# Kernel tuning notes

Measured on AMD Instinct MI355X. Metric: run time of the kernel, lower is better.

The kernel has to match this reference:

```python
import jax, jax.numpy as jnp
import numpy as np

# Concrete segmented-polynomial instance (uniform 1d):
N = 8192      # nodes (rows of input 0 and of the indexed output)
E = 16384     # edges (batch dim of input 1 and of the per-edge product)
S = 16        # segments per operand (buffer_num_segments, same for all 3 operands)
EXT = 64      # operand_extent (uniform segment shape)
P = 2048      # num_paths of the single operation


def setup_inputs() -> dict:
    key = jax.random.key(0)
    k0, k1, k2, k3, k4, k5 = jax.random.split(key, 6)
    x = jax.random.normal(k0, (N, S * EXT), dtype=jnp.float32)          # node features
    y = jax.random.normal(k1, (E, S * EXT), dtype=jnp.float32)          # edge features
    idx_in = jax.random.randint(k2, (E,), 0, N, dtype=jnp.int32)        # gather index for input 0
    idx_out = jax.random.randint(k3, (E,), 0, N, dtype=jnp.int32)       # scatter index for output 0
    path_indices = jax.random.randint(k4, (P, 3), 0, S, dtype=jnp.int32)  # (i_x, j_y, k_out) per path
    path_coefficients = jax.random.normal(k5, (P,), dtype=jnp.float32)
    return {
        "x": x, "y": y,
        "idx_in": idx_in, "idx_out": idx_out,
        "path_indices": path_indices,
        "path_coefficients": path_coefficients,
    }


def reference(x, y, idx_in, idx_out, path_indices, path_coefficients):
    # Dense path-coefficient tensor C[k, i, j]: duplicate paths accumulate,
    # missing (k,i,j) triples are zero. This is the math-dtype (fp32) contraction
    # the uniform-1d kernel performs over segments of equal extent.
    C = jnp.zeros((S, S, S), dtype=x.dtype).at[
        path_indices[:, 2], path_indices[:, 0], path_indices[:, 1]
    ].add(path_coefficients)

    xr = x.reshape(N, S, EXT)[idx_in]   # gather (BATCH_DIM_INDEXED input): [E, S, EXT]
    yr = y.reshape(E, S, EXT)           # batched input:                    [E, S, EXT]

    # out_e[e, k, c] = sum_{i,j} C[k,i,j] * xr[e,i,c] * yr[e,j,c]
    out_e = jnp.einsum('kij,eic,ejc->ekc', C, xr, yr)

    # scatter-add (BATCH_DIM_INDEXED output) into N output rows
    out = jnp.zeros((N, S, EXT), dtype=x.dtype).at[idx_out].add(out_e)
    return out.reshape(N, S * EXT)
```

## Files before the change

### kernel.cpp

```cpp
#include <hip/hip_runtime.h>
#include <hip/hip_bf16.h>

#define N_NODES 8192
#define E_EDGES 16384
#define S_SEG   16
#define EXT     64
#define P_PATHS 2048
#define ROW     (S_SEG * EXT)
#define TE      4

typedef __bf16 bf16x8 __attribute__((ext_vector_type(8)));
typedef float  f32x4  __attribute__((ext_vector_type(4)));
typedef int    int4v  __attribute__((ext_vector_type(4)));

__device__ __forceinline__ int pack_bf16(float a, float b) {
#if __has_builtin(__builtin_amdgcn_cvt_pk_bf16_f32)
    auto r = __builtin_amdgcn_cvt_pk_bf16_f32(a, b);
    return __builtin_bit_cast(int, r);
#else
    unsigned ua = __float_as_uint(a), ub = __float_as_uint(b);
    ua = (ua + 0x7fffu + ((ua >> 16) & 1u)) >> 16;
    ub = (ub + 0x7fffu + ((ub >> 16) & 1u)) & 0xffff0000u;
    return (int)(ua | ub);
#endif
}

__global__ void build_C(const int* __restrict__ pidx,
                        const float* __restrict__ pcoef,
                        unsigned short* __restrict__ Cmat) {
    __shared__ float sC[S_SEG * S_SEG * S_SEG];
    const int tid = threadIdx.x;
    for (int i = tid; i < S_SEG * S_SEG * S_SEG; i += 256) sC[i] = 0.f;
    __syncthreads();
    for (int p = tid; p < P_PATHS; p += 256) {
        int i = pidx[3 * p + 0];
        int j = pidx[3 * p + 1];
        int k = pidx[3 * p + 2];
        atomicAdd(&sC[(k * S_SEG + i) * S_SEG + j], pcoef[p]);
    }
    __syncthreads();
    for (int idx = tid; idx < S_SEG * S_SEG * S_SEG; idx += 256) {
        unsigned u = __float_as_uint(sC[idx]);
        u = (u + 0x7fffu + ((u >> 16) & 1u)) >> 16;
        Cmat[idx] = (unsigned short)u;
    }
}

__global__ __launch_bounds__(256) void seg_poly(
        const float* __restrict__ x, const float* __restrict__ y,
        const int* __restrict__ idx_in, const int* __restrict__ idx_out,
        const unsigned short* __restrict__ Cmat, float* __restrict__ out) {
    __shared__ __attribute__((aligned(16))) float sx[TE][ROW];
    __shared__ __attribute__((aligned(16))) float sy[TE][ROW];

    const int tid  = threadIdx.x;
    const int lane = tid & 63;
    const int wv   = tid >> 6;
    const int quad = lane >> 4;
    const int c    = wv * 16 + (lane & 15);

    int4v afrag[8];
    {
        const int m = lane & 15;
        const unsigned short* base = Cmat + m * 256 + quad * 8;
#pragma unroll
        for (int kk = 0; kk < 8; ++kk)
            afrag[kk] = *(const int4v*)(base + kk * 32);
    }

    const int e0 = blockIdx.x * TE;

#pragma unroll
    for (int t = 0; t < TE; ++t) {
        const int e = e0 + t;
        const float4* xs = (const float4*)(x + (size_t)idx_in[e] * ROW);
        const float4* ys = (const float4*)(y + (size_t)e * ROW);
        ((float4*)sx[t])[tid] = xs[tid];
        ((float4*)sy[t])[tid] = ys[tid];
    }
    __syncthreads();

#pragma unroll
    for (int t = 0; t < TE; ++t) {
        const int e = e0 + t;

        const int jb = (quad & 1) * 8;
        float yv[8];
#pragma unroll
        for (int jr = 0; jr < 8; ++jr) yv[jr] = sy[t][(jb + jr) * EXT + c];

        const int ih = quad >> 1;
        f32x4 acc = {0.f, 0.f, 0.f, 0.f};
#pragma unroll
        for (int kk = 0; kk < 8; ++kk) {
            const float xc = sx[t][(kk * 2 + ih) * EXT + c];
            int4v bi;
            bi[0] = pack_bf16(xc * yv[0], xc * yv[1]);
            bi[1] = pack_bf16(xc * yv[2], xc * yv[3]);
            bi[2] = pack_bf16(xc * yv[4], xc * yv[5]);
            bi[3] = pack_bf16(xc * yv[6], xc * yv[7]);
            acc = __builtin_amdgcn_mfma_f32_16x16x32_bf16(
                __builtin_bit_cast(bf16x8, afrag[kk]),
                __builtin_bit_cast(bf16x8, bi), acc, 0, 0, 0);
        }

        float* ob = out + (size_t)idx_out[e] * ROW;
#pragma unroll
        for (int r = 0; r < 4; ++r)
            atomicAdd(ob + (quad * 4 + r) * EXT + c, acc[r]);
    }
}

extern "C" void kernel_launch(void* const* d_in, const int* in_sizes, int n_in,
                              void* d_out, int out_size, void* d_ws, size_t ws_size,
                              hipStream_t stream) {
    const float* x        = (const float*)d_in[0];
    const float* y        = (const float*)d_in[1];
    const int*   idx_in   = (const int*)d_in[2];
    const int*   idx_out  = (const int*)d_in[3];
    const int*   pidx     = (const int*)d_in[4];
    const float* pcoef    = (const float*)d_in[5];
    float* out            = (float*)d_out;
    unsigned short* Cmat  = (unsigned short*)d_ws;

    hipMemsetAsync(d_out, 0, (size_t)out_size * sizeof(float), stream);

    build_C<<<1, 256, 0, stream>>>(pidx, pcoef, Cmat);
    seg_poly<<<E_EDGES / TE, 256, 0, stream>>>(x, y, idx_in, idx_out, Cmat, out);
}
```

Measured before the change: 182.1 us.

## Replace atomic scatter with CSR-sorted per-node accumulation and fp16 MFMA

```diff
diff --git a/kernel.cpp b/kernel.cpp
--- a/kernel.cpp
+++ b/kernel.cpp
@@ -7,30 +7,26 @@
 #define EXT     64
 #define P_PATHS 2048
 #define ROW     (S_SEG * EXT)
-#define TE      4
 
-typedef __bf16 bf16x8 __attribute__((ext_vector_type(8)));
-typedef float  f32x4  __attribute__((ext_vector_type(4)));
-typedef int    int4v  __attribute__((ext_vector_type(4)));
+typedef _Float16 f16x8  __attribute__((ext_vector_type(8)));
+typedef _Float16 half2v __attribute__((ext_vector_type(2)));
+typedef float    f32x4  __attribute__((ext_vector_type(4)));
 
-__device__ __forceinline__ int pack_bf16(float a, float b) {
-#if __has_builtin(__builtin_amdgcn_cvt_pk_bf16_f32)
-    auto r = __builtin_amdgcn_cvt_pk_bf16_f32(a, b);
-    return __builtin_bit_cast(int, r);
-#else
-    unsigned ua = __float_as_uint(a), ub = __float_as_uint(b);
-    ua = (ua + 0x7fffu + ((ua >> 16) & 1u)) >> 16;
-    ub = (ub + 0x7fffu + ((ub >> 16) & 1u)) & 0xffff0000u;
-    return (int)(ua | ub);
-#endif
-}
+#define WS_CMAT  0
+#define WS_HIST  8192
+#define WS_CURS  40960
+#define WS_ROWS  73728
+#define WS_ELIST 106512
 
-__global__ void build_C(const int* __restrict__ pidx,
-                        const float* __restrict__ pcoef,
-                        unsigned short* __restrict__ Cmat) {
+__global__ void prep(const int* __restrict__ pidx, const float* __restrict__ pcoef,
+                     _Float16* __restrict__ Cmat, int* __restrict__ hist) {
+    const int tid = threadIdx.x;
+    if (blockIdx.x < 32) {
+        hist[blockIdx.x * 256 + tid] = 0;
+        return;
+    }
     __shared__ float sC[S_SEG * S_SEG * S_SEG];
-    const int tid = threadIdx.x;
-    for (int i = tid; i < S_SEG * S_SEG * S_SEG; i += 256) sC[i] = 0.f;
+    for (int i = tid; i < 4096; i += 256) sC[i] = 0.f;
     __syncthreads();
     for (int p = tid; p < P_PATHS; p += 256) {
         int i = pidx[3 * p + 0];
@@ -39,92 +35,148 @@
         atomicAdd(&sC[(k * S_SEG + i) * S_SEG + j], pcoef[p]);
     }
     __syncthreads();
-    for (int idx = tid; idx < S_SEG * S_SEG * S_SEG; idx += 256) {
-        unsigned u = __float_as_uint(sC[idx]);
-        u = (u + 0x7fffu + ((u >> 16) & 1u)) >> 16;
-        Cmat[idx] = (unsigned short)u;
-    }
+    for (int i = tid; i < 4096; i += 256) Cmat[i] = (_Float16)sC[i];
 }
 
-__global__ __launch_bounds__(256) void seg_poly(
+__global__ void hist_k(const int* __restrict__ idx_out, int* __restrict__ hist) {
+    const int e = blockIdx.x * 256 + threadIdx.x;
+    atomicAdd(&hist[idx_out[e]], 1);
+}
+
+__global__ __launch_bounds__(256) void scan_k(const int* __restrict__ hist,
+                                              int* __restrict__ rows,
+                                              int* __restrict__ cursor) {
+    __shared__ int part[256];
+    const int t = threadIdx.x;
+    const int base = t * 32;
+    int loc[32];
+    int s = 0;
+#pragma unroll
+    for (int i = 0; i < 32; ++i) { loc[i] = s; s += hist[base + i]; }
+    part[t] = s;
+    __syncthreads();
+    for (int off = 1; off < 256; off <<= 1) {
+        int v = part[t];
+        int u = (t >= off) ? part[t - off] : 0;
+        __syncthreads();
+        part[t] = v + u;
+        __syncthreads();
+    }
+    const int excl = (t == 0) ? 0 : part[t - 1];
+#pragma unroll
+    for (int i = 0; i < 32; ++i) {
+        int v = excl + loc[i];
+        rows[base + i] = v;
+        cursor[base + i] = v;
+    }
+    if (t == 255) rows[N_NODES] = part[255];
+}
+
+__global__ void scatter_k(const int* __restrict__ idx_out, int* __restrict__ cursor,
+                          int* __restrict__ elist) {
+    const int e = blockIdx.x * 256 + threadIdx.x;
+    const int pos = atomicAdd(&cursor[idx_out[e]], 1);
+    elist[pos] = e;
+}
+
+__global__ __launch_bounds__(256) void seg_poly_node(
         const float* __restrict__ x, const float* __restrict__ y,
-        const int* __restrict__ idx_in, const int* __restrict__ idx_out,
-        const unsigned short* __restrict__ Cmat, float* __restrict__ out) {
-    __shared__ __attribute__((aligned(16))) float sx[TE][ROW];
-    __shared__ __attribute__((aligned(16))) float sy[TE][ROW];
+        const int* __restrict__ idx_in, const _Float16* __restrict__ Cmat,
+        const int* __restrict__ rows, const int* __restrict__ elist,
+        float* __restrict__ out) {
+    __shared__ __attribute__((aligned(16))) _Float16 sxh[ROW];
+    __shared__ __attribute__((aligned(16))) half2v  syp[512];
 
     const int tid  = threadIdx.x;
     const int lane = tid & 63;
     const int wv   = tid >> 6;
     const int quad = lane >> 4;
     const int c    = wv * 16 + (lane & 15);
+    const int n    = blockIdx.x;
 
-    int4v afrag[8];
+    const int beg = rows[n];
+    const int end = rows[n + 1];
+
+    f16x8 afrag[8];
     {
-        const int m = lane & 15;
-        const unsigned short* base = Cmat + m * 256 + quad * 8;
+        const _Float16* basep = Cmat + (lane & 15) * 256 + quad * 8;
 #pragma unroll
         for (int kk = 0; kk < 8; ++kk)
-            afrag[kk] = *(const int4v*)(base + kk * 32);
+            afrag[kk] = *(const f16x8*)(basep + kk * 32);
     }
 
-    const int e0 = blockIdx.x * TE;
+    f32x4 acc = {0.f, 0.f, 0.f, 0.f};
+    const int jb2 = (quad & 1) * 4;
+    const int ih  = quad >> 1;
+
+    for (int p = beg; p < end; ++p) {
+        const int e  = elist[p];
+        const int xr = idx_in[e];
+
+        {
+            const float4 xv = *(const float4*)(x + (size_t)xr * ROW + tid * 4);
+            half2v* sxp = (half2v*)sxh;
+            sxp[tid * 2]     = half2v{(_Float16)xv.x, (_Float16)xv.y};
+            sxp[tid * 2 + 1] = half2v{(_Float16)xv.z, (_Float16)xv.w};
+        }
+        if (tid < 128) {
+            const int jp = tid >> 4;
+            const int cq = (tid & 15) * 4;
+            const float* yb = y + (size_t)e * ROW;
+            const float4 ya = *(const float4*)(yb + (2 * jp) * EXT + cq);
+            const float4 yc = *(const float4*)(yb + (2 * jp + 1) * EXT + cq);
+            syp[jp * 64 + cq + 0] = half2v{(_Float16)ya.x, (_Float16)yc.x};
+            syp[jp * 64 + cq + 1] = half2v{(_Float16)ya.y, (_Float16)yc.y};
+            syp[jp * 64 + cq + 2] = half2v{(_Float16)ya.z, (_Float16)yc.z};
+            syp[jp * 64 + cq + 3] = half2v{(_Float16)ya.w, (_Float16)yc.w};
+        }
+        __syncthreads();
+
+        half2v ypk[4];
+#pragma unroll
+        for (int r = 0; r < 4; ++r) ypk[r] = syp[(jb2 + r) * 64 + c];
 
 #pragma unroll
-    for (int t = 0; t < TE; ++t) {
-        const int e = e0 + t;
-        const float4* xs = (const float4*)(x + (size_t)idx_in[e] * ROW);
-        const float4* ys = (const float4*)(y + (size_t)e * ROW);
-        ((float4*)sx[t])[tid] = xs[tid];
-        ((float4*)sy[t])[tid] = ys[tid];
+        for (int kk = 0; kk < 8; ++kk) {
+            const _Float16 xh = sxh[(2 * kk + ih) * EXT + c];
+            const half2v hx = {xh, xh};
+            const half2v b0 = hx * ypk[0];
+            const half2v b1 = hx * ypk[1];
+            const half2v b2 = hx * ypk[2];
+            const half2v b3 = hx * ypk[3];
+            const f16x8 bfrag = {b0[0], b0[1], b1[0], b1[1], b2[0], b2[1], b3[0], b3[1]};
+            acc = __builtin_amdgcn_mfma_f32_16x16x32_f16(afrag[kk], bfrag, acc, 0, 0, 0);
+        }
+        __syncthreads();
     }
-    __syncthreads();
 
+    float* ob = out + (size_t)n * ROW;
 #pragma unroll
-    for (int t = 0; t < TE; ++t) {
-        const int e = e0 + t;
-
-        const int jb = (quad & 1) * 8;
-        float yv[8];
-#pragma unroll
-        for (int jr = 0; jr < 8; ++jr) yv[jr] = sy[t][(jb + jr) * EXT + c];
-
-        const int ih = quad >> 1;
-        f32x4 acc = {0.f, 0.f, 0.f, 0.f};
-#pragma unroll
-        for (int kk = 0; kk < 8; ++kk) {
-            const float xc = sx[t][(kk * 2 + ih) * EXT + c];
-            int4v bi;
-            bi[0] = pack_bf16(xc * yv[0], xc * yv[1]);
-            bi[1] = pack_bf16(xc * yv[2], xc * yv[3]);
-            bi[2] = pack_bf16(xc * yv[4], xc * yv[5]);
-            bi[3] = pack_bf16(xc * yv[6], xc * yv[7]);
-            acc = __builtin_amdgcn_mfma_f32_16x16x32_bf16(
-                __builtin_bit_cast(bf16x8, afrag[kk]),
-                __builtin_bit_cast(bf16x8, bi), acc, 0, 0, 0);
-        }
-
-        float* ob = out + (size_t)idx_out[e] * ROW;
-#pragma unroll
-        for (int r = 0; r < 4; ++r)
-            atomicAdd(ob + (quad * 4 + r) * EXT + c, acc[r]);
-    }
+    for (int r = 0; r < 4; ++r)
+        ob[(quad * 4 + r) * EXT + c] = acc[r];
 }
 
 extern "C" void kernel_launch(void* const* d_in, const int* in_sizes, int n_in,
                               void* d_out, int out_size, void* d_ws, size_t ws_size,
                               hipStream_t stream) {
-    const float* x        = (const float*)d_in[0];
-    const float* y        = (const float*)d_in[1];
-    const int*   idx_in   = (const int*)d_in[2];
-    const int*   idx_out  = (const int*)d_in[3];
-    const int*   pidx     = (const int*)d_in[4];
-    const float* pcoef    = (const float*)d_in[5];
-    float* out            = (float*)d_out;
-    unsigned short* Cmat  = (unsigned short*)d_ws;
+    const float* x       = (const float*)d_in[0];
+    const float* y       = (const float*)d_in[1];
+    const int*   idx_in  = (const int*)d_in[2];
+    const int*   idx_out = (const int*)d_in[3];
+    const int*   pidx    = (const int*)d_in[4];
+    const float* pcoef   = (const float*)d_in[5];
+    float* out           = (float*)d_out;
 
-    hipMemsetAsync(d_out, 0, (size_t)out_size * sizeof(float), stream);
+    char* ws = (char*)d_ws;
+    _Float16* Cmat = (_Float16*)(ws + WS_CMAT);
+    int* hist      = (int*)(ws + WS_HIST);
+    int* cursor    = (int*)(ws + WS_CURS);
+    int* rows      = (int*)(ws + WS_ROWS);
+    int* elist     = (int*)(ws + WS_ELIST);
 
-    build_C<<<1, 256, 0, stream>>>(pidx, pcoef, Cmat);
-    seg_poly<<<E_EDGES / TE, 256, 0, stream>>>(x, y, idx_in, idx_out, Cmat, out);
+    prep<<<33, 256, 0, stream>>>(pidx, pcoef, Cmat, hist);
+    hist_k<<<E_EDGES / 256, 256, 0, stream>>>(idx_out, hist);
+    scan_k<<<1, 256, 0, stream>>>(hist, rows, cursor);
+    scatter_k<<<E_EDGES / 256, 256, 0, stream>>>(idx_out, cursor, elist);
+    seg_poly_node<<<N_NODES, 256, 0, stream>>>(x, y, idx_in, Cmat, rows, elist, out);
 }
```

After: 169.3 us. 1.08x faster.
